# Performance work log

Hardware: AMD Instinct MI355X
Metric: run time of the kernel (lower is better)

## Reference

```python
import math
import jax, jax.numpy as jnp
import numpy as np

TILE = 128
CAUSAL = True


def setup_inputs() -> dict:
    key = jax.random.key(0)
    kq, kk, kv = jax.random.split(key, 3)
    B, H, T, D = 2, 16, 4096, 64
    query = jax.random.normal(kq, (B, H, T, D), dtype=jnp.float32)
    k = jax.random.normal(kk, (B, H, T, D), dtype=jnp.float32)
    v = jax.random.normal(kv, (B, H, T, D), dtype=jnp.float32)
    return {"query": query, "key": k, "value": v}


def flash_attention(q, k, v, causal=CAUSAL, tile=TILE):
    B, H, T, D = q.shape
    nt = T // tile
    scale = 1.0 / math.sqrt(D)
    # (nt, B, H, tile, D) stacks of key/value tiles
    k_tiles = jnp.moveaxis(k.reshape(B, H, nt, tile, D), 2, 0)
    v_tiles = jnp.moveaxis(v.reshape(B, H, nt, tile, D), 2, 0)
    k_idx_tiles = jnp.arange(T, dtype=jnp.int32).reshape(nt, tile)
    q_idx = jnp.arange(T, dtype=jnp.int32)  # (T,)

    m0 = jnp.full((B, H, T), -jnp.inf, dtype=q.dtype)
    s0 = jnp.zeros((B, H, T), dtype=q.dtype)
    acc0 = jnp.zeros((B, H, T, D), dtype=q.dtype)

    def step(carry, inp):
        m, s, acc = carry
        k_t, v_t, k_idx = inp
        # scores: (B, H, T, tile)
        scores = jnp.einsum('bhqd,bhkd->bhqk', q, k_t) * scale
        if causal:
            mask = k_idx[None, None, None, :] > q_idx[None, None, :, None]
            scores = jnp.where(mask, -jnp.inf, scores)
        tile_max = scores.max(axis=-1)                       # (B,H,T)
        new_m = jnp.maximum(m, tile_max)
        alpha = jnp.exp(m - new_m)                           # (B,H,T)
        p = jnp.exp(scores - new_m[..., None])               # (B,H,T,tile)
        s = s * alpha + p.sum(axis=-1)
        acc = acc * alpha[..., None] + jnp.einsum('bhqk,bhkd->bhqd', p, v_t)
        return (new_m, s, acc), None

    (m, s, acc), _ = jax.lax.scan(step, (m0, s0, acc0), (k_tiles, v_tiles, k_idx_tiles))
    return acc / s[..., None]


def reference(query, key, value):
    return flash_attention(query, key, value)
```

## Files before the change

### kernel.cpp

```cpp
#include <hip/hip_runtime.h>

#define T_SEQ 4096
#define DIM   64
#define NQT   32
#define QTILE 128
#define KTILE 128
#define NBH   32

typedef __attribute__((ext_vector_type(8)))  short bhalf8;
typedef __attribute__((ext_vector_type(16))) float floatx16;

#if __has_builtin(__builtin_amdgcn_exp2f)
#define EXP2F(x) __builtin_amdgcn_exp2f(x)
#else
#define EXP2F(x) exp2f(x)
#endif

__device__ __forceinline__ unsigned pk2bf(float a, float b) {
  unsigned ua = __builtin_bit_cast(unsigned, a) + 0x8000u;
  unsigned ub = __builtin_bit_cast(unsigned, b) + 0x8000u;
  return __builtin_amdgcn_perm(ub, ua, 0x07060302u);
}

union FragU { unsigned u[4]; bhalf8 v; };

__global__ __launch_bounds__(256, 2) void fa_fwd(
    const float* __restrict__ Q, const float* __restrict__ K,
    const float* __restrict__ V, float* __restrict__ O) {
  const int tid  = threadIdx.x;
  const int w    = tid >> 6;
  const int lane = tid & 63;
  const int n    = lane & 31;
  const int h    = lane >> 5;
  const int bid  = blockIdx.x;
  const int bh   = bid & (NBH - 1);
  const int qt   = (NQT - 1) - (bid >> 5);

  const int base = bh * (T_SEQ * DIM);

  __shared__ __align__(16) unsigned short Kl[KTILE * DIM];
  __shared__ __align__(16) unsigned short Vt[DIM * KTILE];

  const int qrow = qt * QTILE + w * 32 + n;
  const float cs = 0.125f * 1.44269504088896340736f;
  FragU qf[4];
  {
    const float* qp = Q + base + qrow * DIM + h * 8;
#pragma unroll
    for (int ks = 0; ks < 4; ++ks) {
      float4 a = *reinterpret_cast<const float4*>(qp + 16 * ks);
      float4 b = *reinterpret_cast<const float4*>(qp + 16 * ks + 4);
      qf[ks].u[0] = pk2bf(a.x * cs, a.y * cs);
      qf[ks].u[1] = pk2bf(a.z * cs, a.w * cs);
      qf[ks].u[2] = pk2bf(b.x * cs, b.y * cs);
      qf[ks].u[3] = pk2bf(b.z * cs, b.w * cs);
    }
  }

  floatx16 o0, o1;
#pragma unroll
  for (int i = 0; i < 16; ++i) { o0[i] = 0.f; o1[i] = 0.f; }
  float m_run = -__builtin_inff();
  float s_run = 0.f;

  for (int kt = 0; kt <= qt; ++kt) {
    __syncthreads();
    {
      const float4* kp4 = reinterpret_cast<const float4*>(K + base + kt * (KTILE * DIM));
      float4 kx[8];
#pragma unroll
      for (int c = 0; c < 8; ++c) kx[c] = kp4[tid + 256 * c];
#pragma unroll
      for (int c = 0; c < 8; ++c) {
        int f4 = tid + 256 * c;
        int kv = f4 >> 4;
        int d0 = (f4 & 15) << 2;
        unsigned lo = pk2bf(kx[c].x, kx[c].y);
        unsigned hi = pk2bf(kx[c].z, kx[c].w);
        unsigned long long u64 = (unsigned long long)lo | ((unsigned long long)hi << 32);
        int idx = (kv << 6) | ((((d0 >> 3) ^ (kv & 7)) << 3) | (d0 & 7));
        *reinterpret_cast<unsigned long long*>(&Kl[idx]) = u64;
      }
      const int kv0 = (tid & 63) << 1;
      const int db  = (tid >> 6) << 4;
      const float* vrow = V + base + kt * (KTILE * DIM) + kv0 * DIM + db;
      float4 va[4], vb[4];
#pragma unroll
      for (int sg = 0; sg < 4; ++sg) {
        va[sg] = *reinterpret_cast<const float4*>(vrow + 4 * sg);
        vb[sg] = *reinterpret_cast<const float4*>(vrow + DIM + 4 * sg);
      }
      const float* vaf = reinterpret_cast<const float*>(va);
      const float* vbf = reinterpret_cast<const float*>(vb);
#pragma unroll
      for (int j = 0; j < 16; ++j) {
        int d = db + j;
        unsigned u = pk2bf(vaf[j], vbf[j]);
        int idx = (d << 7) | ((((kv0 >> 3) ^ (d & 15)) << 3) | (kv0 & 7));
        *reinterpret_cast<unsigned*>(&Vt[idx]) = u;
      }
    }
    __syncthreads();

    floatx16 st[4];
#pragma unroll
    for (int tt = 0; tt < 4; ++tt) {
      floatx16 acc;
#pragma unroll
      for (int i = 0; i < 16; ++i) acc[i] = 0.f;
#pragma unroll
      for (int ks = 0; ks < 4; ++ks) {
        const bhalf8 kfrag = *reinterpret_cast<const bhalf8*>(
            &Kl[((32 * tt + n) << 6) | (((2 * ks + h) ^ (n & 7)) << 3)]);
        acc = __builtin_amdgcn_mfma_f32_32x32x16_bf16(kfrag, qf[ks].v, acc, 0, 0, 0);
      }
      st[tt] = acc;
    }

    if (kt == qt) {
#pragma unroll
      for (int tt = 0; tt < 4; ++tt)
#pragma unroll
        for (int r = 0; r < 16; ++r) {
          int kvloc = 32 * tt + (r & 3) + 8 * (r >> 2) + 4 * h;
          st[tt][r] = (kvloc > 32 * w + n) ? -__builtin_inff() : st[tt][r];
        }
    }

    float rmax = st[0][0];
#pragma unroll
    for (int tt = 0; tt < 4; ++tt)
#pragma unroll
      for (int r = 0; r < 16; ++r) rmax = fmaxf(rmax, st[tt][r]);
    rmax = fmaxf(rmax, __shfl_xor(rmax, 32, 64));
    const float mnew  = fmaxf(m_run, rmax);
    const float alpha = EXP2F(m_run - mnew);
    m_run = mnew;

    float psum = 0.f;
#pragma unroll
    for (int tt = 0; tt < 4; ++tt)
#pragma unroll
      for (int r = 0; r < 16; ++r) {
        float p = EXP2F(st[tt][r] - mnew);
        st[tt][r] = p;
        psum += p;
      }
    psum += __shfl_xor(psum, 32, 64);
    s_run = s_run * alpha + psum;
#pragma unroll
    for (int i = 0; i < 16; ++i) { o0[i] *= alpha; o1[i] *= alpha; }

#pragma unroll
    for (int tt = 0; tt < 4; ++tt) {
      unsigned pk[8];
#pragma unroll
      for (int g = 0; g < 4; ++g) {
        pk[2 * g]     = pk2bf(st[tt][4 * g],     st[tt][4 * g + 1]);
        pk[2 * g + 1] = pk2bf(st[tt][4 * g + 2], st[tt][4 * g + 3]);
      }
      unsigned e0 = (unsigned)__shfl_xor((int)(h ? pk[0] : pk[2]), 32, 64);
      unsigned e1 = (unsigned)__shfl_xor((int)(h ? pk[1] : pk[3]), 32, 64);
      unsigned e2 = (unsigned)__shfl_xor((int)(h ? pk[4] : pk[6]), 32, 64);
      unsigned e3 = (unsigned)__shfl_xor((int)(h ? pk[5] : pk[7]), 32, 64);
      FragU b0, b1;
      b0.u[0] = h ? e0 : pk[0];
      b0.u[1] = h ? e1 : pk[1];
      b0.u[2] = h ? pk[2] : e0;
      b0.u[3] = h ? pk[3] : e1;
      b1.u[0] = h ? e2 : pk[4];
      b1.u[1] = h ? e3 : pk[5];
      b1.u[2] = h ? pk[6] : e2;
      b1.u[3] = h ? pk[7] : e3;

      const int sw = n & 15;
      const bhalf8 v00 = *reinterpret_cast<const bhalf8*>(
          &Vt[(n << 7) | (((4 * tt + 0 + h) ^ sw) << 3)]);
      const bhalf8 v01 = *reinterpret_cast<const bhalf8*>(
          &Vt[(n << 7) | (((4 * tt + 2 + h) ^ sw) << 3)]);
      const bhalf8 v10 = *reinterpret_cast<const bhalf8*>(
          &Vt[((32 + n) << 7) | (((4 * tt + 0 + h) ^ sw) << 3)]);
      const bhalf8 v11 = *reinterpret_cast<const bhalf8*>(
          &Vt[((32 + n) << 7) | (((4 * tt + 2 + h) ^ sw) << 3)]);
      o0 = __builtin_amdgcn_mfma_f32_32x32x16_bf16(v00, b0.v, o0, 0, 0, 0);
      o0 = __builtin_amdgcn_mfma_f32_32x32x16_bf16(v01, b1.v, o0, 0, 0, 0);
      o1 = __builtin_amdgcn_mfma_f32_32x32x16_bf16(v10, b0.v, o1, 0, 0, 0);
      o1 = __builtin_amdgcn_mfma_f32_32x32x16_bf16(v11, b1.v, o1, 0, 0, 0);
    }
  }

  const float inv = 1.0f / s_run;
  float* op = O + base + qrow * DIM;
#pragma unroll
  for (int g = 0; g < 4; ++g) {
    float4 x, y;
    x.x = o0[4 * g] * inv;  x.y = o0[4 * g + 1] * inv;
    x.z = o0[4 * g + 2] * inv;  x.w = o0[4 * g + 3] * inv;
    y.x = o1[4 * g] * inv;  y.y = o1[4 * g + 1] * inv;
    y.z = o1[4 * g + 2] * inv;  y.w = o1[4 * g + 3] * inv;
    *reinterpret_cast<float4*>(op + 8 * g + 4 * h)      = x;
    *reinterpret_cast<float4*>(op + 32 + 8 * g + 4 * h) = y;
  }
}

extern "C" void kernel_launch(void* const* d_in, const int* in_sizes, int n_in,
                              void* d_out, int out_size, void* d_ws, size_t ws_size,
                              hipStream_t stream) {
  (void)in_sizes; (void)n_in; (void)d_ws; (void)ws_size; (void)out_size;
  const float* Q = (const float*)d_in[0];
  const float* K = (const float*)d_in[1];
  const float* V = (const float*)d_in[2];
  float* O = (float*)d_out;
  fa_fwd<<<dim3(NQT * NBH), dim3(256), 0, stream>>>(Q, K, V, O);
}
```

Baseline: 248.2 us.

## Split causal attention into prep, KV-chunked main, and combine kernels

```diff
diff --git a/kernel.cpp b/kernel.cpp
--- a/kernel.cpp
+++ b/kernel.cpp
@@ -6,6 +6,7 @@
 #define QTILE 128
 #define KTILE 128
 #define NBH   32
+#define NCHUNK_TOT 80
 
 typedef __attribute__((ext_vector_type(8)))  short bhalf8;
 typedef __attribute__((ext_vector_type(16))) float floatx16;
@@ -22,11 +23,87 @@
   return __builtin_amdgcn_perm(ub, ua, 0x07060302u);
 }
 
+__device__ __forceinline__ float bflo(unsigned u) {
+  return __builtin_bit_cast(float, u << 16);
+}
+__device__ __forceinline__ float bfhi(unsigned u) {
+  return __builtin_bit_cast(float, u & 0xffff0000u);
+}
+
 union FragU { unsigned u[4]; bhalf8 v; };
 
-__global__ __launch_bounds__(256, 2) void fa_fwd(
-    const float* __restrict__ Q, const float* __restrict__ K,
-    const float* __restrict__ V, float* __restrict__ O) {
+__device__ __forceinline__ void gload_lds16(const void* g, void* l) {
+#if __has_builtin(__builtin_amdgcn_global_load_lds)
+  __builtin_amdgcn_global_load_lds(
+      (const __attribute__((address_space(1))) unsigned*)g,
+      (__attribute__((address_space(3))) unsigned*)l, 16, 0, 0);
+#else
+  *(uint4*)l = *(const uint4*)g;
+#endif
+}
+
+__global__ __launch_bounds__(256, 2) void fa_prep(
+    const float* __restrict__ K, const float* __restrict__ V,
+    unsigned short* __restrict__ Kb, unsigned short* __restrict__ Vb) {
+  const int tid = threadIdx.x;
+  const int bid = blockIdx.x;
+  const int bh = bid >> 5, kt = bid & 31;
+  __shared__ __align__(16) unsigned short SS[16384];
+  unsigned short* Kl = SS;
+  unsigned short* Vt = SS + 8192;
+  const int base = bh * (T_SEQ * DIM) + kt * (KTILE * DIM);
+
+  {
+    const float4* kp4 = reinterpret_cast<const float4*>(K + base);
+    float4 kx[8];
+#pragma unroll
+    for (int c = 0; c < 8; ++c) kx[c] = kp4[tid + 256 * c];
+#pragma unroll
+    for (int c = 0; c < 8; ++c) {
+      int f4 = tid + 256 * c;
+      int kv = f4 >> 4;
+      int d0 = (f4 & 15) << 2;
+      unsigned lo = pk2bf(kx[c].x, kx[c].y);
+      unsigned hi = pk2bf(kx[c].z, kx[c].w);
+      unsigned long long u64 = (unsigned long long)lo | ((unsigned long long)hi << 32);
+      int idx = (kv << 6) | ((((d0 >> 3) ^ (kv & 7)) << 3) | (d0 & 7));
+      *reinterpret_cast<unsigned long long*>(&Kl[idx]) = u64;
+    }
+  }
+  {
+    const int kv0 = (tid & 63) << 1;
+    const int db  = (tid >> 6) << 4;
+    const float* vrow = V + base + kv0 * DIM + db;
+    float4 va[4], vb[4];
+#pragma unroll
+    for (int sg = 0; sg < 4; ++sg) {
+      va[sg] = *reinterpret_cast<const float4*>(vrow + 4 * sg);
+      vb[sg] = *reinterpret_cast<const float4*>(vrow + DIM + 4 * sg);
+    }
+    const float* vaf = reinterpret_cast<const float*>(va);
+    const float* vbf = reinterpret_cast<const float*>(vb);
+#pragma unroll
+    for (int j = 0; j < 16; ++j) {
+      int d = db + j;
+      unsigned u = pk2bf(vaf[j], vbf[j]);
+      int idx = (d << 7) | ((((kv0 >> 3) ^ (d & 15)) << 3) | (kv0 & 7));
+      *reinterpret_cast<unsigned*>(&Vt[idx]) = u;
+    }
+  }
+  __syncthreads();
+  const uint4* S4 = reinterpret_cast<const uint4*>(SS);
+  uint4* KbT = reinterpret_cast<uint4*>(Kb + (size_t)(bh * 32 + kt) * 8192);
+  uint4* VbT = reinterpret_cast<uint4*>(Vb + (size_t)(bh * 32 + kt) * 8192);
+#pragma unroll
+  for (int i = 0; i < 4; ++i) KbT[tid + 256 * i] = S4[tid + 256 * i];
+#pragma unroll
+  for (int i = 0; i < 4; ++i) VbT[tid + 256 * i] = S4[1024 + tid + 256 * i];
+}
+
+__global__ __launch_bounds__(256, 2) void fa_main(
+    const float* __restrict__ Q, const unsigned short* __restrict__ Kb,
+    const unsigned short* __restrict__ Vb,
+    unsigned short* __restrict__ Op, float2* __restrict__ ML) {
   const int tid  = threadIdx.x;
   const int w    = tid >> 6;
   const int lane = tid & 63;
@@ -34,8 +111,16 @@
   const int h    = lane >> 5;
   const int bid  = blockIdx.x;
   const int bh   = bid & (NBH - 1);
-  const int qt   = (NQT - 1) - (bid >> 5);
-
+  const int f    = (NCHUNK_TOT - 1) - (bid >> 5);
+
+  int qt, ch;
+  if (f < 8)       { qt = f;                         ch = 0; }
+  else if (f < 24) { int g = f - 8;  qt = 8  + (g >> 1); ch = g & 1; }
+  else if (f < 48) { int g = f - 24; int q3 = g / 3; qt = 16 + q3; ch = g - 3 * q3; }
+  else             { int g = f - 48; qt = 24 + (g >> 2); ch = g & 3; }
+
+  const int k0   = ch * 8;
+  const int kend = min(k0 + 8, qt + 1);
   const int base = bh * (T_SEQ * DIM);
 
   __shared__ __align__(16) unsigned short Kl[KTILE * DIM];
@@ -63,42 +148,21 @@
   float m_run = -__builtin_inff();
   float s_run = 0.f;
 
-  for (int kt = 0; kt <= qt; ++kt) {
+  const int soff = w * 4096 + lane * 16;
+
+  for (int kt = k0; kt < kend; ++kt) {
     __syncthreads();
     {
-      const float4* kp4 = reinterpret_cast<const float4*>(K + base + kt * (KTILE * DIM));
-      float4 kx[8];
-#pragma unroll
-      for (int c = 0; c < 8; ++c) kx[c] = kp4[tid + 256 * c];
-#pragma unroll
-      for (int c = 0; c < 8; ++c) {
-        int f4 = tid + 256 * c;
-        int kv = f4 >> 4;
-        int d0 = (f4 & 15) << 2;
-        unsigned lo = pk2bf(kx[c].x, kx[c].y);
-        unsigned hi = pk2bf(kx[c].z, kx[c].w);
-        unsigned long long u64 = (unsigned long long)lo | ((unsigned long long)hi << 32);
-        int idx = (kv << 6) | ((((d0 >> 3) ^ (kv & 7)) << 3) | (d0 & 7));
-        *reinterpret_cast<unsigned long long*>(&Kl[idx]) = u64;
-      }
-      const int kv0 = (tid & 63) << 1;
-      const int db  = (tid >> 6) << 4;
-      const float* vrow = V + base + kt * (KTILE * DIM) + kv0 * DIM + db;
-      float4 va[4], vb[4];
-#pragma unroll
-      for (int sg = 0; sg < 4; ++sg) {
-        va[sg] = *reinterpret_cast<const float4*>(vrow + 4 * sg);
-        vb[sg] = *reinterpret_cast<const float4*>(vrow + DIM + 4 * sg);
-      }
-      const float* vaf = reinterpret_cast<const float*>(va);
-      const float* vbf = reinterpret_cast<const float*>(vb);
-#pragma unroll
-      for (int j = 0; j < 16; ++j) {
-        int d = db + j;
-        unsigned u = pk2bf(vaf[j], vbf[j]);
-        int idx = (d << 7) | ((((kv0 >> 3) ^ (d & 15)) << 3) | (kv0 & 7));
-        *reinterpret_cast<unsigned*>(&Vt[idx]) = u;
-      }
+      const char* kb = reinterpret_cast<const char*>(Kb) + (size_t)((bh << 5) + kt) * 16384;
+      const char* vb = reinterpret_cast<const char*>(Vb) + (size_t)((bh << 5) + kt) * 16384;
+      char* kl = reinterpret_cast<char*>(Kl);
+      char* vl = reinterpret_cast<char*>(Vt);
+#pragma unroll
+      for (int r = 0; r < 4; ++r)
+        gload_lds16(kb + soff + r * 1024, kl + soff + r * 1024);
+#pragma unroll
+      for (int r = 0; r < 4; ++r)
+        gload_lds16(vb + soff + r * 1024, vl + soff + r * 1024);
     }
     __syncthreads();
 
@@ -189,6 +253,231 @@
     }
   }
 
+  const int pidx = (((bh << 5) | qt) << 2) | ch;
+  unsigned* opr = reinterpret_cast<unsigned*>(Op) + (size_t)pidx * 4096 + (w * 32 + n) * 32;
+#pragma unroll
+  for (int g = 0; g < 4; ++g) {
+    opr[4 * g + 2 * h]          = pk2bf(o0[4 * g],     o0[4 * g + 1]);
+    opr[4 * g + 2 * h + 1]      = pk2bf(o0[4 * g + 2], o0[4 * g + 3]);
+    opr[16 + 4 * g + 2 * h]     = pk2bf(o1[4 * g],     o1[4 * g + 1]);
+    opr[16 + 4 * g + 2 * h + 1] = pk2bf(o1[4 * g + 2], o1[4 * g + 3]);
+  }
+  if (h == 0) ML[(pidx << 7) + w * 32 + n] = make_float2(m_run, s_run);
+}
+
+__global__ __launch_bounds__(256, 2) void fa_combine(
+    const unsigned short* __restrict__ Op, const float2* __restrict__ ML,
+    float* __restrict__ O) {
+  const int bid = blockIdx.x;
+  const int bh = bid >> 5, qt = bid & 31;
+  const int nch = (qt >> 3) + 1;
+  const int t = threadIdx.x;
+  const int r = t >> 1, half = t & 1;
+  const int pbase = ((bh << 5) | qt) << 2;
+
+  float m[4], l[4];
+  for (int i = 0; i < nch; ++i) {
+    float2 x = ML[((pbase + i) << 7) + r];
+    m[i] = x.x; l[i] = x.y;
+  }
+  float M = m[0];
+  for (int i = 1; i < nch; ++i) M = fmaxf(M, m[i]);
+
+  float acc[32];
+#pragma unroll
+  for (int j = 0; j < 32; ++j) acc[j] = 0.f;
+  float L = 0.f;
+
+  for (int i = 0; i < nch; ++i) {
+    float wgt = EXP2F(m[i] - M);
+    L += wgt * l[i];
+    const uint4* p = reinterpret_cast<const uint4*>(
+        Op + (size_t)(pbase + i) * 8192 + r * 64 + 32 * half);
+    uint4 q4[4];
+#pragma unroll
+    for (int j = 0; j < 4; ++j) q4[j] = p[j];
+    const unsigned* u = reinterpret_cast<const unsigned*>(q4);
+#pragma unroll
+    for (int j = 0; j < 16; ++j) {
+      acc[2 * j]     += wgt * bflo(u[j]);
+      acc[2 * j + 1] += wgt * bfhi(u[j]);
+    }
+  }
+  const float inv = 1.0f / L;
+  float* op = O + (size_t)bh * (T_SEQ * DIM) + (size_t)(qt * 128 + r) * DIM + 32 * half;
+#pragma unroll
+  for (int g = 0; g < 8; ++g) {
+    float4 x;
+    x.x = acc[4 * g] * inv;  x.y = acc[4 * g + 1] * inv;
+    x.z = acc[4 * g + 2] * inv;  x.w = acc[4 * g + 3] * inv;
+    *reinterpret_cast<float4*>(op + 4 * g) = x;
+  }
+}
+
+__global__ __launch_bounds__(256, 2) void fa_mono(
+    const float* __restrict__ Q, const float* __restrict__ K,
+    const float* __restrict__ V, float* __restrict__ O) {
+  const int tid  = threadIdx.x;
+  const int w    = tid >> 6;
+  const int lane = tid & 63;
+  const int n    = lane & 31;
+  const int h    = lane >> 5;
+  const int bid  = blockIdx.x;
+  const int bh   = bid & (NBH - 1);
+  const int qt   = (NQT - 1) - (bid >> 5);
+
+  const int base = bh * (T_SEQ * DIM);
+  __shared__ __align__(16) unsigned short Kl[KTILE * DIM];
+  __shared__ __align__(16) unsigned short Vt[DIM * KTILE];
+
+  const int qrow = qt * QTILE + w * 32 + n;
+  const float cs = 0.125f * 1.44269504088896340736f;
+  FragU qf[4];
+  {
+    const float* qp = Q + base + qrow * DIM + h * 8;
+#pragma unroll
+    for (int ks = 0; ks < 4; ++ks) {
+      float4 a = *reinterpret_cast<const float4*>(qp + 16 * ks);
+      float4 b = *reinterpret_cast<const float4*>(qp + 16 * ks + 4);
+      qf[ks].u[0] = pk2bf(a.x * cs, a.y * cs);
+      qf[ks].u[1] = pk2bf(a.z * cs, a.w * cs);
+      qf[ks].u[2] = pk2bf(b.x * cs, b.y * cs);
+      qf[ks].u[3] = pk2bf(b.z * cs, b.w * cs);
+    }
+  }
+
+  floatx16 o0, o1;
+#pragma unroll
+  for (int i = 0; i < 16; ++i) { o0[i] = 0.f; o1[i] = 0.f; }
+  float m_run = -__builtin_inff();
+  float s_run = 0.f;
+
+  for (int kt = 0; kt <= qt; ++kt) {
+    __syncthreads();
+    {
+      const float4* kp4 = reinterpret_cast<const float4*>(K + base + kt * (KTILE * DIM));
+      float4 kx[8];
+#pragma unroll
+      for (int c = 0; c < 8; ++c) kx[c] = kp4[tid + 256 * c];
+#pragma unroll
+      for (int c = 0; c < 8; ++c) {
+        int f4 = tid + 256 * c;
+        int kv = f4 >> 4;
+        int d0 = (f4 & 15) << 2;
+        unsigned lo = pk2bf(kx[c].x, kx[c].y);
+        unsigned hi = pk2bf(kx[c].z, kx[c].w);
+        unsigned long long u64 = (unsigned long long)lo | ((unsigned long long)hi << 32);
+        int idx = (kv << 6) | ((((d0 >> 3) ^ (kv & 7)) << 3) | (d0 & 7));
+        *reinterpret_cast<unsigned long long*>(&Kl[idx]) = u64;
+      }
+      const int kv0 = (tid & 63) << 1;
+      const int db  = (tid >> 6) << 4;
+      const float* vrow = V + base + kt * (KTILE * DIM) + kv0 * DIM + db;
+      float4 va[4], vb[4];
+#pragma unroll
+      for (int sg = 0; sg < 4; ++sg) {
+        va[sg] = *reinterpret_cast<const float4*>(vrow + 4 * sg);
+        vb[sg] = *reinterpret_cast<const float4*>(vrow + DIM + 4 * sg);
+      }
+      const float* vaf = reinterpret_cast<const float*>(va);
+      const float* vbf = reinterpret_cast<const float*>(vb);
+#pragma unroll
+      for (int j = 0; j < 16; ++j) {
+        int d = db + j;
+        unsigned u = pk2bf(vaf[j], vbf[j]);
+        int idx = (d << 7) | ((((kv0 >> 3) ^ (d & 15)) << 3) | (kv0 & 7));
+        *reinterpret_cast<unsigned*>(&Vt[idx]) = u;
+      }
+    }
+    __syncthreads();
+
+    floatx16 st[4];
+#pragma unroll
+    for (int tt = 0; tt < 4; ++tt) {
+      floatx16 acc;
+#pragma unroll
+      for (int i = 0; i < 16; ++i) acc[i] = 0.f;
+#pragma unroll
+      for (int ks = 0; ks < 4; ++ks) {
+        const bhalf8 kfrag = *reinterpret_cast<const bhalf8*>(
+            &Kl[((32 * tt + n) << 6) | (((2 * ks + h) ^ (n & 7)) << 3)]);
+        acc = __builtin_amdgcn_mfma_f32_32x32x16_bf16(kfrag, qf[ks].v, acc, 0, 0, 0);
+      }
+      st[tt] = acc;
+    }
+
+    if (kt == qt) {
+#pragma unroll
+      for (int tt = 0; tt < 4; ++tt)
+#pragma unroll
+        for (int r = 0; r < 16; ++r) {
+          int kvloc = 32 * tt + (r & 3) + 8 * (r >> 2) + 4 * h;
+          st[tt][r] = (kvloc > 32 * w + n) ? -__builtin_inff() : st[tt][r];
+        }
+    }
+
+    float rmax = st[0][0];
+#pragma unroll
+    for (int tt = 0; tt < 4; ++tt)
+#pragma unroll
+      for (int r = 0; r < 16; ++r) rmax = fmaxf(rmax, st[tt][r]);
+    rmax = fmaxf(rmax, __shfl_xor(rmax, 32, 64));
+    const float mnew  = fmaxf(m_run, rmax);
+    const float alpha = EXP2F(m_run - mnew);
+    m_run = mnew;
+
+    float psum = 0.f;
+#pragma unroll
+    for (int tt = 0; tt < 4; ++tt)
+#pragma unroll
+      for (int r = 0; r < 16; ++r) {
+        float p = EXP2F(st[tt][r] - mnew);
+        st[tt][r] = p;
+        psum += p;
+      }
+    psum += __shfl_xor(psum, 32, 64);
+    s_run = s_run * alpha + psum;
+#pragma unroll
+    for (int i = 0; i < 16; ++i) { o0[i] *= alpha; o1[i] *= alpha; }
+
+#pragma unroll
+    for (int tt = 0; tt < 4; ++tt) {
+      unsigned pk[8];
+#pragma unroll
+      for (int g = 0; g < 4; ++g) {
+        pk[2 * g]     = pk2bf(st[tt][4 * g],     st[tt][4 * g + 1]);
+        pk[2 * g + 1] = pk2bf(st[tt][4 * g + 2], st[tt][4 * g + 3]);
+      }
+      unsigned e0 = (unsigned)__shfl_xor((int)(h ? pk[0] : pk[2]), 32, 64);
+      unsigned e1 = (unsigned)__shfl_xor((int)(h ? pk[1] : pk[3]), 32, 64);
+      unsigned e2 = (unsigned)__shfl_xor((int)(h ? pk[4] : pk[6]), 32, 64);
+      unsigned e3 = (unsigned)__shfl_xor((int)(h ? pk[5] : pk[7]), 32, 64);
+      FragU b0, b1;
+      b0.u[0] = h ? e0 : pk[0];
+      b0.u[1] = h ? e1 : pk[1];
+      b0.u[2] = h ? pk[2] : e0;
+      b0.u[3] = h ? pk[3] : e1;
+      b1.u[0] = h ? e2 : pk[4];
+      b1.u[1] = h ? e3 : pk[5];
+      b1.u[2] = h ? pk[6] : e2;
+      b1.u[3] = h ? pk[7] : e3;
+
+      const int sw = n & 15;
+      const bhalf8 v00 = *reinterpret_cast<const bhalf8*>(
+          &Vt[(n << 7) | (((4 * tt + 0 + h) ^ sw) << 3)]);
+      const bhalf8 v01 = *reinterpret_cast<const bhalf8*>(
+          &Vt[(n << 7) | (((4 * tt + 2 + h) ^ sw) << 3)]);
+      const bhalf8 v10 = *reinterpret_cast<const bhalf8*>(
+          &Vt[((32 + n) << 7) | (((4 * tt + 0 + h) ^ sw) << 3)]);
+      const bhalf8 v11 = *reinterpret_cast<const bhalf8*>(
+          &Vt[((32 + n) << 7) | (((4 * tt + 2 + h) ^ sw) << 3)]);
+      o0 = __builtin_amdgcn_mfma_f32_32x32x16_bf16(v00, b0.v, o0, 0, 0, 0);
+      o0 = __builtin_amdgcn_mfma_f32_32x32x16_bf16(v01, b1.v, o0, 0, 0, 0);
+      o1 = __builtin_amdgcn_mfma_f32_32x32x16_bf16(v10, b0.v, o1, 0, 0, 0);
+      o1 = __builtin_amdgcn_mfma_f32_32x32x16_bf16(v11, b1.v, o1, 0, 0, 0);
+    }
+  }
+
   const float inv = 1.0f / s_run;
   float* op = O + base + qrow * DIM;
 #pragma unroll
@@ -206,10 +495,27 @@
 extern "C" void kernel_launch(void* const* d_in, const int* in_sizes, int n_in,
                               void* d_out, int out_size, void* d_ws, size_t ws_size,
                               hipStream_t stream) {
-  (void)in_sizes; (void)n_in; (void)d_ws; (void)ws_size; (void)out_size;
+  (void)in_sizes; (void)n_in; (void)out_size;
   const float* Q = (const float*)d_in[0];
   const float* K = (const float*)d_in[1];
   const float* V = (const float*)d_in[2];
   float* O = (float*)d_out;
-  fa_fwd<<<dim3(NQT * NBH), dim3(256), 0, stream>>>(Q, K, V, O);
-}
+
+  const size_t OFF_KB = 0;
+  const size_t OFF_VB = 16777216;
+  const size_t OFF_OP = 33554432;
+  const size_t OFF_ML = 100663296;
+  const size_t NEED   = 104857600;
+
+  if (ws_size >= NEED) {
+    unsigned short* Kb = (unsigned short*)((char*)d_ws + OFF_KB);
+    unsigned short* Vb = (unsigned short*)((char*)d_ws + OFF_VB);
+    unsigned short* Op = (unsigned short*)((char*)d_ws + OFF_OP);
+    float2*         ML = (float2*)((char*)d_ws + OFF_ML);
+    fa_prep<<<dim3(NBH * NQT), dim3(256), 0, stream>>>(K, V, Kb, Vb);
+    fa_main<<<dim3(NBH * NCHUNK_TOT), dim3(256), 0, stream>>>(Q, Kb, Vb, Op, ML);
+    fa_combine<<<dim3(NBH * NQT), dim3(256), 0, stream>>>(Op, ML, O);
+  } else {
+    fa_mono<<<dim3(NQT * NBH), dim3(256), 0, stream>>>(Q, K, V, O);
+  }
+}
```

Measured after the change: 250.7 us. About the same (+1.0%).
